# Performance work log

Measured on AMD Instinct MI355X. Metric: run time of the kernel, lower is better.

## Reference

```python
import jax, jax.numpy as jnp
import numpy as np

ALPHA = 32.0 ** 2
EPS = 1e-5
SCALE = 64 ** (-0.5)  # dim_head ** -0.5
HEADS = 8


def stable_softmax(t, alpha=ALPHA):
    t = t / alpha
    t = t - jax.lax.stop_gradient(jnp.max(t, axis=-1, keepdims=True))
    return jax.nn.softmax(t * alpha, axis=-1)


def setup_inputs() -> dict:
    key = jax.random.key(0)
    k1, k2, k3 = jax.random.split(key, 3)
    dim, inner = 512, 8 * 64
    x = jax.random.normal(k1, (8, dim, 32, 32), dtype=jnp.float32)
    gamma = jnp.ones((1, dim, 1, 1), dtype=jnp.float32)
    # conv2d 1x1 weights, stored as [out_ch, in_ch]
    w_qkv = jax.random.normal(k2, (inner * 3, dim), dtype=jnp.float32) * (dim ** -0.5)
    w_out = jax.random.normal(k3, (dim, inner), dtype=jnp.float32) * (inner ** -0.5)
    return {"x": x, "gamma": gamma, "w_qkv": w_qkv, "w_out": w_out}


def reference(x, gamma, w_qkv, w_out):
    b, c, H, W = x.shape
    residual = x
    # LayerNormChan: normalize over channel dim (biased variance), scale by gamma
    mean = jnp.mean(x, axis=1, keepdims=True)
    var = jnp.var(x, axis=1, keepdims=True)
    xn = (x - mean) / jnp.sqrt(var + EPS) * gamma
    # 1x1 conv QKV projection
    qkv = jnp.einsum('oc,bchw->bohw', w_qkv, xn)
    q, k, v = jnp.split(qkv, 3, axis=1)
    n = H * W
    def to_heads(t):
        return t.reshape(b, HEADS, -1, n)  # b h c (x y)
    q, k, v = map(to_heads, (q, k, v))
    sim = jnp.einsum('bhci,bhcj->bhij', q, k) * SCALE
    attn = stable_softmax(sim)
    out = jnp.einsum('bhij,bhcj->bhci', attn, v)
    out = out.reshape(b, -1, H, W)  # b (h c) x y
    out = jnp.einsum('oc,bchw->bohw', w_out, out)
    return out + residual
```

## Files before the change

### kernel.cpp

```cpp
#include <hip/hip_runtime.h>
#include <hip/hip_bf16.h>

#define NDIM   512
#define NPOS   1024
#define NB     8
#define INNER  1536
#define DHEAD  64

typedef __attribute__((ext_vector_type(8))) short bf8v;
typedef __attribute__((ext_vector_type(4))) float f4v;

__device__ __forceinline__ f4v mfma16(bf8v a, bf8v b, f4v c) {
    return __builtin_amdgcn_mfma_f32_16x16x32_bf16(a, b, c, 0, 0, 0);
}

__device__ __forceinline__ unsigned short f2bs(float v) {
    __hip_bfloat16 h = __float2bfloat16(v);
    return *reinterpret_cast<unsigned short*>(&h);
}

__device__ __forceinline__ void gl_lds16(const unsigned short* g, unsigned short* l) {
    __builtin_amdgcn_global_load_lds(
        (const __attribute__((address_space(1))) void*)g,
        (__attribute__((address_space(3))) void*)l,
        16, 0, 0);
}

__global__ __launch_bounds__(256) void prep_kernel(
    const float* __restrict__ x, const float* __restrict__ gamma,
    const float* __restrict__ wq, const float* __restrict__ wo,
    unsigned short* __restrict__ xnT, unsigned short* __restrict__ wqb,
    unsigned short* __restrict__ wob)
{
    const int blk = blockIdx.x;
    const int t = threadIdx.x;
    if (blk >= 256) {
        const int n1 = INNER * NDIM / 4;
        int i = (blk - 256) * 256 + t;
        const float* src; unsigned short* dst; int j;
        if (i < n1) { src = wq; dst = wqb; j = i; }
        else        { src = wo; dst = wob; j = i - n1; }
        float4 v = ((const float4*)src)[j];
        ushort4 u;
        u.x = f2bs(v.x); u.y = f2bs(v.y); u.z = f2bs(v.z); u.w = f2bs(v.w);
        ((ushort4*)dst)[j] = u;
        return;
    }
    __shared__ float ssum[8][32];
    __shared__ float ssq[8][32];
    __shared__ float mean_s[32];
    __shared__ float rstd_s[32];
    __shared__ unsigned short tile[32][72];

    const int b = blk >> 5;
    const int n0 = (blk & 31) * 32;
    {
        const int ln = t & 31, cg = t >> 5;
        const float* xp = x + (size_t)b * NDIM * NPOS + n0 + ln;
        float s = 0.f, ss = 0.f;
#pragma unroll 8
        for (int c = cg * 64; c < cg * 64 + 64; ++c) {
            float v = xp[(size_t)c * NPOS];
            s += v; ss += v * v;
        }
        ssum[cg][ln] = s; ssq[cg][ln] = ss;
    }
    __syncthreads();
    if (t < 32) {
        float st = 0.f, sq = 0.f;
#pragma unroll
        for (int g = 0; g < 8; ++g) { st += ssum[g][t]; sq += ssq[g][t]; }
        float m = st * (1.0f / NDIM);
        float var = sq * (1.0f / NDIM) - m * m;
        mean_s[t] = m;
        rstd_s[t] = rsqrtf(var + 1e-5f);
    }
    __syncthreads();

    const int cl = t >> 2, nq = (t & 3) * 8;
    const int nr = t >> 3, ch = (t & 7) * 8;
    for (int c0 = 0; c0 < NDIM; c0 += 64) {
        const float g = gamma[c0 + cl];
        const float* xp = x + ((size_t)b * NDIM + c0 + cl) * NPOS + n0 + nq;
        float4 v0 = *(const float4*)(xp);
        float4 v1 = *(const float4*)(xp + 4);
        float4 m0 = *(const float4*)&mean_s[nq];
        float4 m1 = *(const float4*)&mean_s[nq + 4];
        float4 r0 = *(const float4*)&rstd_s[nq];
        float4 r1 = *(const float4*)&rstd_s[nq + 4];
        tile[nq + 0][cl] = f2bs((v0.x - m0.x) * r0.x * g);
        tile[nq + 1][cl] = f2bs((v0.y - m0.y) * r0.y * g);
        tile[nq + 2][cl] = f2bs((v0.z - m0.z) * r0.z * g);
        tile[nq + 3][cl] = f2bs((v0.w - m0.w) * r0.w * g);
        tile[nq + 4][cl] = f2bs((v1.x - m1.x) * r1.x * g);
        tile[nq + 5][cl] = f2bs((v1.y - m1.y) * r1.y * g);
        tile[nq + 6][cl] = f2bs((v1.z - m1.z) * r1.z * g);
        tile[nq + 7][cl] = f2bs((v1.w - m1.w) * r1.w * g);
        __syncthreads();
        unsigned short* dst = xnT + ((size_t)b * NPOS + n0 + nr) * NDIM + c0 + ch;
        *(uint4*)dst = *(const uint4*)&tile[nr][ch];
        __syncthreads();
    }
}

__global__ __launch_bounds__(256) void qkv_mfma_kernel(
    const unsigned short* __restrict__ wq, const unsigned short* __restrict__ xnT,
    unsigned short* __restrict__ qT, unsigned short* __restrict__ kT,
    unsigned short* __restrict__ vv)
{
    __shared__ __align__(16) unsigned short smem[3 * 8192];

    const int b = blockIdx.z;
    const int m0 = blockIdx.y * 128, n0 = blockIdx.x * 128;
    const int t = threadIdx.x, w = t >> 6, lane = t & 63;
    const int l15 = lane & 15, quad = lane >> 4;
    const int wm = (w >> 1) * 64, wn = (w & 1) * 64;
    const unsigned short* Abase = wq + (size_t)m0 * NDIM;
    const unsigned short* Bbase = xnT + ((size_t)b * NPOS + n0) * NDIM;

    const int rl = lane >> 2, sl = lane & 3;
    const int cw = (sl ^ ((rl >> 1) & 3)) * 8;
    const int sA = (quad ^ ((l15 >> 1) & 3)) * 8;

    f4v acc[4][4];
#pragma unroll
    for (int i = 0; i < 4; ++i)
#pragma unroll
        for (int j = 0; j < 4; ++j) { acc[i][j][0]=0.f; acc[i][j][1]=0.f; acc[i][j][2]=0.f; acc[i][j][3]=0.f; }

    auto STAGE = [&](int k0, unsigned short* buf) {
#pragma unroll
        for (int e = 0; e < 2; ++e) {
            const int seg = w * 2 + e;
            const int r = seg * 16 + rl;
            gl_lds16(Abase + (size_t)r * NDIM + k0 + cw, buf + seg * 512);
            gl_lds16(Bbase + (size_t)r * NDIM + k0 + cw, buf + 4096 + seg * 512);
        }
    };

    STAGE(0, smem);
    STAGE(32, smem + 8192);

#pragma unroll
    for (int kt = 0; kt < 16; ++kt) {
        if (kt < 15) asm volatile("s_waitcnt vmcnt(4)" ::: "memory");
        else         asm volatile("s_waitcnt vmcnt(0)" ::: "memory");
        __builtin_amdgcn_sched_barrier(0);
        __builtin_amdgcn_s_barrier();
        __builtin_amdgcn_sched_barrier(0);
        if (kt + 2 < 16) STAGE((kt + 2) * 32, smem + ((kt + 2) % 3) * 8192);
        unsigned short* At = smem + (kt % 3) * 8192;
        unsigned short* Bt = At + 4096;
        bf8v af[4], bfr[4];
#pragma unroll
        for (int ms = 0; ms < 4; ++ms) af[ms]  = *(const bf8v*)&At[(wm + ms * 16 + l15) * 32 + sA];
#pragma unroll
        for (int ns = 0; ns < 4; ++ns) bfr[ns] = *(const bf8v*)&Bt[(wn + ns * 16 + l15) * 32 + sA];
#pragma unroll
        for (int ms = 0; ms < 4; ++ms)
#pragma unroll
            for (int ns = 0; ns < 4; ++ns)
                acc[ms][ns] = mfma16(af[ms], bfr[ns], acc[ms][ns]);
    }
    __syncthreads();

    const int sec = m0 >> 9;
    const int om  = m0 & 511;
    if (sec == 2) {
        unsigned short (*bw)[72] = (unsigned short(*)[72])(smem + w * 64 * 72);
        unsigned short* vbase = vv + ((size_t)b * NDIM + om) * NPOS + n0;
#pragma unroll
        for (int ms = 0; ms < 4; ++ms)
#pragma unroll
            for (int ns = 0; ns < 4; ++ns)
#pragma unroll
                for (int r = 0; r < 4; ++r)
                    bw[ms * 16 + quad * 4 + r][ns * 16 + l15] = f2bs(acc[ms][ns][r]);
#pragma unroll
        for (int r2 = 0; r2 < 4; ++r2) {
            const int ml = r2 * 16 + (lane >> 2);
            unsigned short* dstr = vbase + (size_t)(wm + ml) * NPOS + wn + (lane & 3) * 8;
            *(uint4*)dstr        = *(const uint4*)&bw[ml][(lane & 3) * 8];
            *(uint4*)(dstr + 32) = *(const uint4*)&bw[ml][32 + (lane & 3) * 8];
        }
    } else {
        const float qsc = (sec == 0) ? 0.18033688f : 1.0f;
        unsigned short* gT = (sec == 0 ? qT : kT) + ((size_t)b * NPOS + n0) * NDIM + om;
        unsigned short (*bw)[72] = (unsigned short(*)[72])(smem + w * 64 * 72);
#pragma unroll
        for (int ms = 0; ms < 4; ++ms)
#pragma unroll
            for (int ns = 0; ns < 4; ++ns)
#pragma unroll
                for (int r = 0; r < 4; ++r)
                    bw[ns * 16 + l15][ms * 16 + quad * 4 + r] = f2bs(acc[ms][ns][r] * qsc);
#pragma unroll
        for (int r2 = 0; r2 < 4; ++r2) {
            const int nl = r2 * 16 + (lane >> 2);
            unsigned short* dstr = gT + (size_t)(wn + nl) * NDIM + wm + (lane & 3) * 8;
            *(uint4*)dstr        = *(const uint4*)&bw[nl][(lane & 3) * 8];
            *(uint4*)(dstr + 32) = *(const uint4*)&bw[nl][32 + (lane & 3) * 8];
        }
    }
}

__global__ __launch_bounds__(256, 2) void attn_mfma8_kernel(
    const unsigned short* __restrict__ qT, const unsigned short* __restrict__ kT,
    const unsigned short* __restrict__ vv, unsigned short* __restrict__ attnT)
{
    __shared__ __align__(16) unsigned short Kb[2][4096];
    __shared__ __align__(16) unsigned short Vb[2][4096];
    __shared__ __align__(16) unsigned short Ps[4][32][72];

    const int blk = blockIdx.x;
    const int xg = blk & 7, rr = blk >> 3;
    const int i0 = (rr & 7) * 128;
    const int bh = ((rr >> 3) << 3) | xg;
    const int b = bh >> 3, h = bh & 7;

    const int t = threadIdx.x, w = t >> 6, lane = t & 63;
    const int l15 = lane & 15, quad = lane >> 4;

    const unsigned short* kbase = kT + (size_t)b * NPOS * NDIM + h * DHEAD;
    const unsigned short* vbase = vv + ((size_t)b * NDIM + h * DHEAD) * NPOS;

    bf8v bq[2][2];
#pragma unroll
    for (int g = 0; g < 2; ++g) {
        const unsigned short* qrow =
            qT + ((size_t)b * NPOS + i0 + w * 32 + g * 16 + l15) * NDIM + h * DHEAD;
        bq[g][0] = *(const bf8v*)(qrow + quad * 8);
        bq[g][1] = *(const bf8v*)(qrow + 32 + quad * 8);
    }

    bf8v bones;
#pragma unroll
    for (int e = 0; e < 8; ++e) bones[e] = (short)0x3F80;

    const int rloc = lane >> 3;
    const int gch = ((lane & 7) ^ (rloc & 7)) * 8;
    const int sw0 = (quad ^ (l15 & 7)) * 8;
    const int sw1 = ((4 + quad) ^ (l15 & 7)) * 8;

#pragma unroll
    for (int e = 0; e < 2; ++e) {
        const int seg = w * 2 + e;
        const int row = seg * 8 + rloc;
        gl_lds16(kbase + (size_t)row * NDIM + gch, &Kb[0][seg * 512]);
        gl_lds16(vbase + (size_t)row * NPOS + gch, &Vb[0][seg * 512]);
    }

    f4v oc[2][5];
#pragma unroll
    for (int mg = 0; mg < 2; ++mg)
#pragma unroll
        for (int cs = 0; cs < 5; ++cs) { oc[mg][cs][0]=0.f; oc[mg][cs][1]=0.f; oc[mg][cs][2]=0.f; oc[mg][cs][3]=0.f; }

#pragma unroll 2
    for (int j0 = 0; j0 < NPOS; j0 += 64) {
        const int cur = (j0 >> 6) & 1, nxt = cur ^ 1;
        __syncthreads();
        if (j0 + 64 < NPOS) {
#pragma unroll
            for (int e = 0; e < 2; ++e) {
                const int seg = w * 2 + e;
                const int row = seg * 8 + rloc;
                gl_lds16(kbase + (size_t)(j0 + 64 + row) * NDIM + gch, &Kb[nxt][seg * 512]);
                gl_lds16(vbase + (size_t)row * NPOS + j0 + 64 + gch, &Vb[nxt][seg * 512]);
            }
        }

        f4v sacc[4][2];
        __builtin_amdgcn_s_setprio(1);
#pragma unroll
        for (int jt = 0; jt < 4; ++jt) {
            const int krow = (jt * 16 + l15) * 64;
            bf8v ak0 = *(const bf8v*)&Kb[cur][krow + sw0];
            bf8v ak1 = *(const bf8v*)&Kb[cur][krow + sw1];
#pragma unroll
            for (int g = 0; g < 2; ++g) {
                f4v s; s[0]=0.f; s[1]=0.f; s[2]=0.f; s[3]=0.f;
                s = mfma16(ak0, bq[g][0], s);
                sacc[jt][g] = mfma16(ak1, bq[g][1], s);
            }
        }
        __builtin_amdgcn_s_setprio(0);

#pragma unroll
        for (int jt = 0; jt < 4; ++jt)
#pragma unroll
            for (int g = 0; g < 2; ++g) {
                ushort4 pu;
                pu.x = f2bs(__builtin_amdgcn_exp2f(sacc[jt][g][0]));
                pu.y = f2bs(__builtin_amdgcn_exp2f(sacc[jt][g][1]));
                pu.z = f2bs(__builtin_amdgcn_exp2f(sacc[jt][g][2]));
                pu.w = f2bs(__builtin_amdgcn_exp2f(sacc[jt][g][3]));
                *(ushort4*)&Ps[w][g * 16 + l15][jt * 16 + quad * 4] = pu;
            }

        bf8v ap[2][2];
#pragma unroll
        for (int mg = 0; mg < 2; ++mg) {
            ap[mg][0] = *(const bf8v*)&Ps[w][mg * 16 + l15][quad * 8];
            ap[mg][1] = *(const bf8v*)&Ps[w][mg * 16 + l15][32 + quad * 8];
        }
        __builtin_amdgcn_s_setprio(1);
#pragma unroll
        for (int cs = 0; cs < 4; ++cs) {
            const int vrow = (cs * 16 + l15) * 64;
            bf8v bv0 = *(const bf8v*)&Vb[cur][vrow + sw0];
            bf8v bv1 = *(const bf8v*)&Vb[cur][vrow + sw1];
#pragma unroll
            for (int mg = 0; mg < 2; ++mg) {
                oc[mg][cs] = mfma16(ap[mg][0], bv0, oc[mg][cs]);
                oc[mg][cs] = mfma16(ap[mg][1], bv1, oc[mg][cs]);
            }
        }
#pragma unroll
        for (int mg = 0; mg < 2; ++mg) {
            oc[mg][4] = mfma16(ap[mg][0], bones, oc[mg][4]);
            oc[mg][4] = mfma16(ap[mg][1], bones, oc[mg][4]);
        }
        __builtin_amdgcn_s_setprio(0);
    }

#pragma unroll
    for (int mg = 0; mg < 2; ++mg) {
        float inv[4];
#pragma unroll
        for (int r = 0; r < 4; ++r) inv[r] = __builtin_amdgcn_rcpf(oc[mg][4][r]);
#pragma unroll
        for (int cs = 0; cs < 4; ++cs)
#pragma unroll
            for (int r = 0; r < 4; ++r)
                Ps[w][mg * 16 + quad * 4 + r][cs * 16 + l15] = f2bs(oc[mg][cs][r] * inv[r]);
    }
    {
        const int br = lane >> 1;
        const int bc = lane & 1;
        unsigned short* dst =
            attnT + ((size_t)b * NPOS + i0 + w * 32 + br) * NDIM + h * DHEAD;
#pragma unroll
        for (int q2 = 0; q2 < 4; ++q2)
            *(uint4*)(dst + (q2 * 2 + bc) * 8) = *(const uint4*)&Ps[w][br][(q2 * 2 + bc) * 8];
    }
}

__global__ __launch_bounds__(256) void out_mfma_kernel(
    const unsigned short* __restrict__ wo, const unsigned short* __restrict__ attnT,
    const float* __restrict__ x, float* __restrict__ outp)
{
    __shared__ __align__(16) unsigned short smem[3 * 6144];

    const int b = blockIdx.z;
    const int m0 = blockIdx.y * 64, n0 = blockIdx.x * 128;
    const int t = threadIdx.x, w = t >> 6, lane = t & 63;
    const int l15 = lane & 15, quad = lane >> 4;
    const int wm = (w >> 1) * 32, wn = (w & 1) * 64;
    const unsigned short* Abase = wo + (size_t)m0 * NDIM;
    const unsigned short* Bbase = attnT + ((size_t)b * NPOS + n0) * NDIM;

    const int rl = lane >> 2, sl = lane & 3;
    const int cw = (sl ^ ((rl >> 1) & 3)) * 8;
    const int sA = (quad ^ ((l15 >> 1) & 3)) * 8;

    f4v acc[2][4];
#pragma unroll
    for (int i = 0; i < 2; ++i)
#pragma unroll
        for (int j = 0; j < 4; ++j) { acc[i][j][0]=0.f; acc[i][j][1]=0.f; acc[i][j][2]=0.f; acc[i][j][3]=0.f; }

    auto STAGE = [&](int k0, unsigned short* buf) {
        const int r = w * 16 + rl;
        gl_lds16(Abase + (size_t)r * NDIM + k0 + cw, buf + w * 512);
#pragma unroll
        for (int e = 0; e < 2; ++e) {
            const int seg = w * 2 + e;
            const int rb = seg * 16 + rl;
            gl_lds16(Bbase + (size_t)rb * NDIM + k0 + cw, buf + 2048 + seg * 512);
        }
    };

    STAGE(0, smem);
    STAGE(32, smem + 6144);

#pragma unroll
    for (int kt = 0; kt < 16; ++kt) {
        if (kt < 15) asm volatile("s_waitcnt vmcnt(3)" ::: "memory");
        else         asm volatile("s_waitcnt vmcnt(0)" ::: "memory");
        __builtin_amdgcn_sched_barrier(0);
        __builtin_amdgcn_s_barrier();
        __builtin_amdgcn_sched_barrier(0);
        if (kt + 2 < 16) STAGE((kt + 2) * 32, smem + ((kt + 2) % 3) * 6144);
        unsigned short* At = smem + (kt % 3) * 6144;
        unsigned short* Bt = At + 2048;
        bf8v af[2], bfr[4];
#pragma unroll
        for (int ms = 0; ms < 2; ++ms) af[ms]  = *(const bf8v*)&At[(wm + ms * 16 + l15) * 32 + sA];
#pragma unroll
        for (int ns = 0; ns < 4; ++ns) bfr[ns] = *(const bf8v*)&Bt[(wn + ns * 16 + l15) * 32 + sA];
#pragma unroll
        for (int ms = 0; ms < 2; ++ms)
#pragma unroll
            for (int ns = 0; ns < 4; ++ns)
                acc[ms][ns] = mfma16(af[ms], bfr[ns], acc[ms][ns]);
    }
    const float* xb = x + ((size_t)b * NDIM + m0) * NPOS + n0;
    float* ob = outp + ((size_t)b * NDIM + m0) * NPOS + n0;
#pragma unroll
    for (int ms = 0; ms < 2; ++ms)
#pragma unroll
        for (int r = 0; r < 4; ++r) {
            int m = wm + ms * 16 + quad * 4 + r;
#pragma unroll
            for (int ns = 0; ns < 4; ++ns) {
                int n = wn + ns * 16 + l15;
                ob[(size_t)m * NPOS + n] = acc[ms][ns][r] + xb[(size_t)m * NPOS + n];
            }
        }
}

extern "C" void kernel_launch(void* const* d_in, const int* in_sizes, int n_in,
                              void* d_out, int out_size, void* d_ws, size_t ws_size,
                              hipStream_t stream) {
    const float* x     = (const float*)d_in[0];
    const float* gamma = (const float*)d_in[1];
    const float* w_qkv = (const float*)d_in[2];
    const float* w_out = (const float*)d_in[3];
    float* out = (float*)d_out;

    unsigned short* xnT = (unsigned short*)d_ws;
    unsigned short* wqb = xnT + (size_t)NB * NPOS * NDIM;
    unsigned short* wob = wqb + (size_t)INNER * NDIM;
    unsigned short* qTw = wob + (size_t)NDIM * NDIM;
    unsigned short* kTw = qTw + (size_t)NB * NPOS * NDIM;
    unsigned short* vvw = kTw + (size_t)NB * NPOS * NDIM;
    unsigned short* aTw = vvw + (size_t)NB * NPOS * NDIM;

    prep_kernel<<<256 + (INNER * NDIM + NDIM * NDIM) / 4 / 256, 256, 0, stream>>>(
        x, gamma, w_qkv, w_out, xnT, wqb, wob);
    qkv_mfma_kernel<<<dim3(NPOS / 128, INNER / 128, NB), 256, 0, stream>>>(
        wqb, xnT, qTw, kTw, vvw);
    attn_mfma8_kernel<<<512, 256, 0, stream>>>(qTw, kTw, vvw, aTw);
    out_mfma_kernel<<<dim3(NPOS / 128, NDIM / 64, NB), 256, 0, stream>>>(wob, aTw, x, out);
}
```

Baseline: 132.1 us.

## Triple-buffer K/V loads in attention kernel and raise priority around MFMA loops

The attention kernel's K/V staging goes from double to triple buffering. Loads are issued two tiles ahead, with an explicit vmcnt wait and barrier replacing the __syncthreads, so global-to-LDS latency overlaps more compute. Both GEMM kernels also wrap their MFMA inner loops in s_setprio to favor matrix issue. Triple buffering raises LDS use per block, which may limit occupancy under the launch_bounds of 2 blocks.

```diff
diff --git a/kernel.cpp b/kernel.cpp
--- a/kernel.cpp
+++ b/kernel.cpp
@@ -156,11 +156,13 @@
         for (int ms = 0; ms < 4; ++ms) af[ms]  = *(const bf8v*)&At[(wm + ms * 16 + l15) * 32 + sA];
 #pragma unroll
         for (int ns = 0; ns < 4; ++ns) bfr[ns] = *(const bf8v*)&Bt[(wn + ns * 16 + l15) * 32 + sA];
+        __builtin_amdgcn_s_setprio(1);
 #pragma unroll
         for (int ms = 0; ms < 4; ++ms)
 #pragma unroll
             for (int ns = 0; ns < 4; ++ns)
                 acc[ms][ns] = mfma16(af[ms], bfr[ns], acc[ms][ns]);
+        __builtin_amdgcn_s_setprio(0);
     }
     __syncthreads();
 
@@ -208,8 +210,8 @@
     const unsigned short* __restrict__ qT, const unsigned short* __restrict__ kT,
     const unsigned short* __restrict__ vv, unsigned short* __restrict__ attnT)
 {
-    __shared__ __align__(16) unsigned short Kb[2][4096];
-    __shared__ __align__(16) unsigned short Vb[2][4096];
+    __shared__ __align__(16) unsigned short Kb[3][4096];
+    __shared__ __align__(16) unsigned short Vb[3][4096];
     __shared__ __align__(16) unsigned short Ps[4][32][72];
 
     const int blk = blockIdx.x;
@@ -242,13 +244,18 @@
     const int sw0 = (quad ^ (l15 & 7)) * 8;
     const int sw1 = ((4 + quad) ^ (l15 & 7)) * 8;
 
-#pragma unroll
-    for (int e = 0; e < 2; ++e) {
-        const int seg = w * 2 + e;
-        const int row = seg * 8 + rloc;
-        gl_lds16(kbase + (size_t)row * NDIM + gch, &Kb[0][seg * 512]);
-        gl_lds16(vbase + (size_t)row * NPOS + gch, &Vb[0][seg * 512]);
-    }
+    auto STAGEKV = [&](int j0, int bi) {
+#pragma unroll
+        for (int e = 0; e < 2; ++e) {
+            const int seg = w * 2 + e;
+            const int row = seg * 8 + rloc;
+            gl_lds16(kbase + (size_t)(j0 + row) * NDIM + gch, &Kb[bi][seg * 512]);
+            gl_lds16(vbase + (size_t)row * NPOS + j0 + gch, &Vb[bi][seg * 512]);
+        }
+    };
+
+    STAGEKV(0, 0);
+    STAGEKV(64, 1);
 
     f4v oc[2][5];
 #pragma unroll
@@ -257,18 +264,14 @@
         for (int cs = 0; cs < 5; ++cs) { oc[mg][cs][0]=0.f; oc[mg][cs][1]=0.f; oc[mg][cs][2]=0.f; oc[mg][cs][3]=0.f; }
 
 #pragma unroll 2
-    for (int j0 = 0; j0 < NPOS; j0 += 64) {
-        const int cur = (j0 >> 6) & 1, nxt = cur ^ 1;
-        __syncthreads();
-        if (j0 + 64 < NPOS) {
-#pragma unroll
-            for (int e = 0; e < 2; ++e) {
-                const int seg = w * 2 + e;
-                const int row = seg * 8 + rloc;
-                gl_lds16(kbase + (size_t)(j0 + 64 + row) * NDIM + gch, &Kb[nxt][seg * 512]);
-                gl_lds16(vbase + (size_t)row * NPOS + j0 + 64 + gch, &Vb[nxt][seg * 512]);
-            }
-        }
+    for (int kt = 0; kt < 16; ++kt) {
+        if (kt < 15) asm volatile("s_waitcnt vmcnt(4)" ::: "memory");
+        else         asm volatile("s_waitcnt vmcnt(0)" ::: "memory");
+        __builtin_amdgcn_sched_barrier(0);
+        __builtin_amdgcn_s_barrier();
+        __builtin_amdgcn_sched_barrier(0);
+        if (kt + 2 < 16) STAGEKV((kt + 2) * 64, (kt + 2) % 3);
+        const int cur = kt % 3;
 
         f4v sacc[4][2];
         __builtin_amdgcn_s_setprio(1);
@@ -399,11 +402,13 @@
         for (int ms = 0; ms < 2; ++ms) af[ms]  = *(const bf8v*)&At[(wm + ms * 16 + l15) * 32 + sA];
 #pragma unroll
         for (int ns = 0; ns < 4; ++ns) bfr[ns] = *(const bf8v*)&Bt[(wn + ns * 16 + l15) * 32 + sA];
+        __builtin_amdgcn_s_setprio(1);
 #pragma unroll
         for (int ms = 0; ms < 2; ++ms)
 #pragma unroll
             for (int ns = 0; ns < 4; ++ns)
                 acc[ms][ns] = mfma16(af[ms], bfr[ns], acc[ms][ns]);
+        __builtin_amdgcn_s_setprio(0);
     }
     const float* xb = x + ((size_t)b * NDIM + m0) * NPOS + n0;
     float* ob = outp + ((size_t)b * NDIM + m0) * NPOS + n0;
```

Result: no change. 133.0 us (+0.7%).
